# Optimization experiments

Measured on AMD Instinct MI355X. Metric: run time of the kernel, lower is better.

## Reference

```python
import jax, jax.numpy as jnp
import numpy as np

B = 8192
G = 30            # max_grid_size
C = 10            # num_colors
IN = G * G * C    # 9000 encoder input
HID = 128         # encoder hidden
ADIM = 128        # answer_dim
ZDIM = 64         # latent_dim
GF = 16           # grid_feature_dim
RHID = 64         # refiner / selector hidden
NT = 64           # num_templates
T = 3             # num_cycles
TAU = 1.0         # gumbel-softmax temperature


def _gelu(x):
    return jax.nn.gelu(x, approximate=False)  # torch nn.GELU default = exact erf


def setup_inputs() -> dict:
    key = jax.random.key(0)
    ks = jax.random.split(key, 32)
    s = 0.02
    inp = {
        "grid": jax.random.randint(ks[0], (B, G, G), 0, C, dtype=jnp.int64),
        "grid_features": jax.random.normal(ks[1], (B, GF), jnp.float32),
        "gumbel": jax.random.gumbel(ks[2], (B, NT), jnp.float32),
        # encoder (TinyMLPMixer)
        "enc_w1": jax.random.normal(ks[3], (IN, HID), jnp.float32) * s,
        "enc_b1": jnp.zeros((HID,), jnp.float32),
        "enc_w2": jax.random.normal(ks[4], (HID, HID), jnp.float32) * s,
        "enc_b2": jnp.zeros((HID,), jnp.float32),
        "wy": jax.random.normal(ks[5], (HID, ADIM), jnp.float32) * s,
        "by": jnp.zeros((ADIM,), jnp.float32),
        "wz": jax.random.normal(ks[6], (HID, ZDIM), jnp.float32) * s,
        "bz": jnp.zeros((ZDIM,), jnp.float32),
        # refine_z: [y,z,gf] (208) -> 64 -> ZDIM
        "rz_w1": jax.random.normal(ks[7], (ADIM + ZDIM + GF, RHID), jnp.float32) * s,
        "rz_b1": jnp.zeros((RHID,), jnp.float32),
        "rz_w2": jax.random.normal(ks[8], (RHID, ZDIM), jnp.float32) * s,
        "rz_b2": jnp.zeros((ZDIM,), jnp.float32),
        # refine_y: [z,y,gf] (208) -> 64 -> ADIM
        "ry_w1": jax.random.normal(ks[9], (ZDIM + ADIM + GF, RHID), jnp.float32) * s,
        "ry_b1": jnp.zeros((RHID,), jnp.float32),
        "ry_w2": jax.random.normal(ks[10], (RHID, ADIM), jnp.float32) * s,
        "ry_b2": jnp.zeros((ADIM,), jnp.float32),
        # formula selector: ADIM -> 64 -> NT
        "sel_w1": jax.random.normal(ks[11], (ADIM, RHID), jnp.float32) * s,
        "sel_b1": jnp.zeros((RHID,), jnp.float32),
        "sel_w2": jax.random.normal(ks[12], (RHID, NT), jnp.float32) * s,
        "sel_b2": jnp.zeros((NT,), jnp.float32),
    }
    return inp


def _mlp2(x, w1, b1, w2, b2):
    return _gelu(x @ w1 + b1) @ w2 + b2


def reference(grid, grid_features, gumbel,
              enc_w1, enc_b1, enc_w2, enc_b2, wy, by, wz, bz,
              rz_w1, rz_b1, rz_w2, rz_b2, ry_w1, ry_b1, ry_w2, ry_b2,
              sel_w1, sel_b1, sel_w2, sel_b2):
    # --- TinyMLPMixer encoder ---
    x = jax.nn.one_hot(grid, C, dtype=jnp.float32).reshape(grid.shape[0], -1)  # [B, 9000]
    h = _gelu(x @ enc_w1 + enc_b1)
    h = _gelu(h @ enc_w2 + enc_b2)
    y = h @ wy + by   # [B, ADIM]
    z = h @ wz + bz   # [B, ZDIM]

    def refine_z(y, z):
        return _mlp2(jnp.concatenate([y, z, grid_features], axis=-1), rz_w1, rz_b1, rz_w2, rz_b2)

    def refine_y(y, z):
        return _mlp2(jnp.concatenate([z, y, grid_features], axis=-1), ry_w1, ry_b1, ry_w2, ry_b2)

    # --- recursive refinement: T-1 no-grad cycles, final cycle with grads ---
    for _ in range(T - 1):
        z = jax.lax.stop_gradient(refine_z(y, z))
        y = jax.lax.stop_gradient(refine_y(y, z))
    z = refine_z(y, z)
    y = refine_y(y, z)

    # --- TinyFormulaSelector (Gumbel-Softmax, soft, noise passed in) ---
    logits = _mlp2(y, sel_w1, sel_b1, sel_w2, sel_b2)  # [B, NT]
    selection = jax.nn.softmax((logits + gumbel) / TAU, axis=-1)
    return selection
```

## Files before the change

kernel.cpp:

```cpp
#include <hip/hip_runtime.h>

typedef _Float16 f16;
typedef f16 h8 __attribute__((ext_vector_type(8)));
typedef float f32x4 __attribute__((ext_vector_type(4)));
typedef unsigned int uint;
typedef unsigned char uchar;

#define BM 32
#define KS_E 284
#define CSTR 920

#define SH 136
#define SAZ 232
#define SLOG 68

#define N_W1B (8*KS_E*512)
#define OW2   0
#define OWY   16384
#define OWZ   32768
#define ORZ1  40960
#define ORZ2  55296
#define ORY1  59392
#define ORY2  73728
#define OS1   81920
#define OS2   90112
#define N_SMH 94208

__device__ __forceinline__ float geluf(float x){
  return 0.5f * x * (1.0f + erff(x * 0.70710678118654752f));
}

#define MFMA16(a,b,c) __builtin_amdgcn_mfma_f32_16x16x32_f16(a, b, c, 0, 0, 0)

__device__ __forceinline__ f32x4 mfma8(uint2 a, uint2 b, f32x4 c){
  union { uint2 u; long long l; } ua, ub;
  ua.u = a; ub.u = b;
  return __builtin_amdgcn_mfma_f32_16x16x32_fp8_fp8(ua.l, ub.l, c, 0, 0, 0);
}

__device__ __forceinline__ f32x4 mfma_tile(const f16* __restrict__ act, int strideH,
                                           const f16* __restrict__ Wbase,
                                           int nks, f32x4 acc, int lane){
  #pragma unroll
  for (int ks = 0; ks < nks; ++ks){
    h8 a = *(const h8*)(act + (lane&15)*strideH + ks*32 + (lane>>4)*8);
    h8 b = *(const h8*)(Wbase + ks*512 + lane*8);
    acc = MFMA16(a, b, acc);
  }
  return acc;
}

__device__ __forceinline__ f32x4 cinit(const float* __restrict__ bias, int Nb, int lane){
  float v = bias[Nb + (lane&15)];
  f32x4 c; c[0]=v; c[1]=v; c[2]=v; c[3]=v;
  return c;
}

__device__ __forceinline__ void storeC16(f16* __restrict__ dst, int stride, int Nb,
                                         f32x4 c, int lane, bool dogelu){
  int col = Nb + (lane&15);
  int r0  = (lane>>4)*4;
  #pragma unroll
  for (int r = 0; r < 4; ++r){
    float v = c[r];
    if (dogelu) v = geluf(v);
    dst[(r0+r)*stride + col] = (f16)v;
  }
}

__global__ void prep_kernel(const float* __restrict__ w1,
  const float* __restrict__ w2, const float* __restrict__ wy, const float* __restrict__ wz,
  const float* __restrict__ rz1, const float* __restrict__ rz2,
  const float* __restrict__ ry1, const float* __restrict__ ry2,
  const float* __restrict__ sel1, const float* __restrict__ sel2, f16* __restrict__ ws)
{
  int idx = blockIdx.x * 256 + threadIdx.x;
  uchar* w8 = (uchar*)ws;
  if (idx < 9000*128){
    int row = idx >> 7;
    int n   = idx & 127;
    int p   = row / 10;
    int c   = row - p*10;
    int k   = 904*c + p;
    int nt  = n >> 4;
    int ks  = k >> 5;
    int lane = (((k>>3)&3)<<4) | (n&15);
    uint pk = __builtin_amdgcn_cvt_pk_fp8_f32(w1[idx], 0.f, 0, false);
    w8[((size_t)(nt*KS_E + ks)<<9) + (lane<<3) + (k&7)] = (uchar)(pk & 255u);
    return;
  }
  int i2 = idx - 9000*128;
  if (i2 < 11264){
    int k, n;
    if (i2 < 5120){
      int c = i2 >> 9, rest = i2 & 511;
      k = 904*c + 900 + (rest >> 7);
      n = rest & 127;
    } else {
      int j = i2 - 5120;
      k = 9040 + (j >> 7);
      n = j & 127;
    }
    int nt = n >> 4, ks = k >> 5;
    int lane = (((k>>3)&3)<<4) | (n&15);
    w8[((size_t)(nt*KS_E + ks)<<9) + (lane<<3) + (k&7)] = (uchar)0;
    return;
  }
  int r = i2 - 11264;
  if (r >= N_SMH) return;
  f16* smw = (f16*)(w8 + N_W1B);
  const float* src; int Ksrc, N, KS, off, perm = 0;
  if      (r < OWY) { src=w2;   Ksrc=128; N=128; KS=4; off=OW2; }
  else if (r < OWZ) { src=wy;   Ksrc=128; N=128; KS=4; off=OWY; }
  else if (r < ORZ1){ src=wz;   Ksrc=128; N=64;  KS=4; off=OWZ; }
  else if (r < ORZ2){ src=rz1;  Ksrc=208; N=64;  KS=7; off=ORZ1; }
  else if (r < ORY1){ src=rz2;  Ksrc=64;  N=64;  KS=2; off=ORZ2; }
  else if (r < ORY2){ src=ry1;  Ksrc=208; N=64;  KS=7; off=ORY1; perm=1; }
  else if (r < OS1) { src=ry2;  Ksrc=64;  N=128; KS=2; off=ORY2; }
  else if (r < OS2) { src=sel1; Ksrc=128; N=64;  KS=4; off=OS1; }
  else              { src=sel2; Ksrc=64;  N=64;  KS=2; off=OS2; }
  int l    = r - off;
  int e    = l & 7;
  int lane = (l >> 3) & 63;
  int frag = l >> 9;
  int kst  = frag % KS;
  int nt   = frag / KS;
  int k    = kst*32 + (lane>>4)*8 + e;
  int o    = nt*16 + (lane&15);
  float v = 0.f;
  if (perm){
    int sr = (k < 128) ? 64 + k : (k < 192) ? k - 128 : (k < 208) ? k : -1;
    if (sr >= 0) v = src[sr*N + o];
  } else if (k < Ksrc) v = src[k*N + o];
  smw[r] = (f16)v;
}

extern "C" __global__ __launch_bounds__(512, 1) void enc_kernel(
  const int* __restrict__ grd, const float* __restrict__ b1,
  const f16* __restrict__ ws, f16* hbuf)
{
  __shared__ __align__(16) char colL[32*CSTR];

  const int t  = threadIdx.x;
  const int s0 = blockIdx.x * BM;
  const int lane = t & 63;
  const int w    = t >> 6;

  {
    const uint4* gv = (const uint4*)(grd + (size_t)s0 * 900);
    #pragma unroll
    for (int it = 0; it < 15; ++it){
      int idx4 = it*512 + t;
      if (idx4 < 7200){
        uint4 v = gv[idx4];
        uint pk = (v.x & 255u) | ((v.y & 255u) << 8) | ((v.z & 255u) << 16) | ((v.w & 255u) << 24);
        uint s  = (uint)(idx4 * 9321u) >> 21;
        uint p4 = (uint)idx4 - s * 225u;
        *(uint*)(colL + s*CSTR + p4*4) = pk;
      }
    }
  }
  __syncthreads();

  const char* colRowA = colL + (lane & 15) * CSTR;
  const char* colRowB = colRowA + 16 * CSTR;
  const char* Wp = (const char*)ws + (size_t)(w * KS_E) * 512 + lane*8;

  f32x4 acc0 = {0.f,0.f,0.f,0.f};
  f32x4 acc1 = {0.f,0.f,0.f,0.f};

  uint2 q0 = *(const uint2*)(Wp);
  uint2 q1 = *(const uint2*)(Wp + 512);
  uint2 q2 = *(const uint2*)(Wp + 1024);
  uint2 q3 = *(const uint2*)(Wp + 1536);
  uint k0 = (uint)((lane >> 4) * 8);

#define ESTEP(Q, PFIDX) { \
    uint q = k0 >> 3; \
    uint c = (q * 2320u) >> 18; \
    uint p0 = (q - 113u * c) << 3; \
    uint2 wvA = *(const uint2*)(colRowA + p0); \
    uint2 wvB = *(const uint2*)(colRowB + p0); \
    uint cc4 = c * 0x01010101u; \
    uint2 a0, a1; \
    a0.x = (0x10101010u - (wvA.x ^ cc4)) & 0x10101010u; \
    a0.y = (0x10101010u - (wvA.y ^ cc4)) & 0x10101010u; \
    a1.x = (0x10101010u - (wvB.x ^ cc4)) & 0x10101010u; \
    a1.y = (0x10101010u - (wvB.y ^ cc4)) & 0x10101010u; \
    acc0 = mfma8(a0, Q, acc0); \
    acc1 = mfma8(a1, Q, acc1); \
    Q = *(const uint2*)(Wp + (size_t)(PFIDX)*512); \
    k0 += 32; }
#define ETAIL(Q) { \
    uint q = k0 >> 3; \
    uint c = (q * 2320u) >> 18; \
    uint p0 = (q - 113u * c) << 3; \
    uint2 wvA = *(const uint2*)(colRowA + p0); \
    uint2 wvB = *(const uint2*)(colRowB + p0); \
    uint cc4 = c * 0x01010101u; \
    uint2 a0, a1; \
    a0.x = (0x10101010u - (wvA.x ^ cc4)) & 0x10101010u; \
    a0.y = (0x10101010u - (wvA.y ^ cc4)) & 0x10101010u; \
    a1.x = (0x10101010u - (wvB.x ^ cc4)) & 0x10101010u; \
    a1.y = (0x10101010u - (wvB.y ^ cc4)) & 0x10101010u; \
    acc0 = mfma8(a0, Q, acc0); \
    acc1 = mfma8(a1, Q, acc1); \
    k0 += 32; }

  #pragma unroll 2
  for (int it = 0; it < 70; ++it){
    ESTEP(q0, it*4 + 4)
    ESTEP(q1, it*4 + 5)
    ESTEP(q2, it*4 + 6)
    ESTEP(q3, it*4 + 7)
  }
  ETAIL(q0) ETAIL(q1) ETAIL(q2) ETAIL(q3)
#undef ESTEP
#undef ETAIL

  {
    int col = w*16 + (lane & 15);
    float bb = b1[col];
    int r0 = (lane >> 4) * 4;
    #pragma unroll
    for (int r = 0; r < 4; ++r){
      hbuf[(size_t)(s0 + r0 + r)*128 + col]      = (f16)geluf(acc0[r]*32.0f + bb);
      hbuf[(size_t)(s0 + 16 + r0 + r)*128 + col] = (f16)geluf(acc1[r]*32.0f + bb);
    }
  }
}

extern "C" __global__ __launch_bounds__(256, 2) void phases_kernel(
  const float* __restrict__ gfeat, const float* __restrict__ gum,
  const float* __restrict__ b2, const float* __restrict__ by, const float* __restrict__ bz,
  const float* __restrict__ rzb1, const float* __restrict__ rzb2,
  const float* __restrict__ ryb1, const float* __restrict__ ryb2,
  const float* __restrict__ sb1, const float* __restrict__ sb2,
  const f16* __restrict__ ws, const f16* hbuf, float* out)
{
  __shared__ __align__(16) f16 Hb[16*SH];
  __shared__ __align__(16) f16 Bb[16*SH];
  __shared__ __align__(16) f16 Az[16*SAZ];
  __shared__ __align__(16) float Lb[16*SLOG];

  const int t  = threadIdx.x;
  const int s0 = blockIdx.x * 16;
  const int lane  = t & 63;
  const int ns    = t >> 6;
  const int slane = t >> 4;
  const int flane = t & 15;

  {
    h8 hv = *(const h8*)(hbuf + (size_t)s0*128 + t*8);
    *(h8*)(Hb + (t>>4)*SH + (t&15)*8) = hv;
    Az[slane*SAZ + 192 + flane] = (f16)gfeat[(size_t)(s0 + slane)*16 + flane];
    Az[slane*SAZ + 208 + flane] = (f16)0.f;
  }
  __syncthreads();

  const f16* SMW = (const f16*)((const char*)ws + N_W1B);

  {
    f32x4 c0 = cinit(b2, ns*32,      lane);
    f32x4 c1 = cinit(b2, ns*32 + 16, lane);
    c0 = mfma_tile(Hb, SH, SMW + OW2 + (ns*2+0)*4*512, 4, c0, lane);
    c1 = mfma_tile(Hb, SH, SMW + OW2 + (ns*2+1)*4*512, 4, c1, lane);
    storeC16(Bb, SH, ns*32,      c0, lane, true);
    storeC16(Bb, SH, ns*32 + 16, c1, lane, true);
  }
  __syncthreads();

  {
    f32x4 y0 = cinit(by, ns*32,      lane);
    f32x4 y1 = cinit(by, ns*32 + 16, lane);
    f32x4 z0 = cinit(bz, ns*16,      lane);
    y0 = mfma_tile(Bb, SH, SMW + OWY + (ns*2+0)*4*512, 4, y0, lane);
    y1 = mfma_tile(Bb, SH, SMW + OWY + (ns*2+1)*4*512, 4, y1, lane);
    z0 = mfma_tile(Bb, SH, SMW + OWZ + ns*4*512,       4, z0, lane);
    storeC16(Az, SAZ, ns*32,       y0, lane, false);
    storeC16(Az, SAZ, ns*32 + 16,  y1, lane, false);
    storeC16(Az, SAZ, 128 + ns*16, z0, lane, false);
  }
  __syncthreads();

  #pragma unroll 1
  for (int cyc = 0; cyc < 3; ++cyc){
    {
      f32x4 h0 = cinit(rzb1, ns*16, lane);
      h0 = mfma_tile(Az, SAZ, SMW + ORZ1 + ns*7*512, 7, h0, lane);
      storeC16(Bb, SH, ns*16, h0, lane, true);
    }
    __syncthreads();
    {
      f32x4 z = cinit(rzb2, ns*16, lane);
      z = mfma_tile(Bb, SH, SMW + ORZ2 + ns*2*512, 2, z, lane);
      storeC16(Az, SAZ, 128 + ns*16, z, lane, false);
    }
    __syncthreads();
    {
      f32x4 h1 = cinit(ryb1, ns*16, lane);
      h1 = mfma_tile(Az, SAZ, SMW + ORY1 + ns*7*512, 7, h1, lane);
      storeC16(Bb, SH, ns*16, h1, lane, true);
    }
    __syncthreads();
    {
      f32x4 y0 = cinit(ryb2, ns*32,      lane);
      f32x4 y1 = cinit(ryb2, ns*32 + 16, lane);
      y0 = mfma_tile(Bb, SH, SMW + ORY2 + (ns*2+0)*2*512, 2, y0, lane);
      y1 = mfma_tile(Bb, SH, SMW + ORY2 + (ns*2+1)*2*512, 2, y1, lane);
      storeC16(Az, SAZ, ns*32,      y0, lane, false);
      storeC16(Az, SAZ, ns*32 + 16, y1, lane, false);
    }
    __syncthreads();
  }

  {
    f32x4 s1 = cinit(sb1, ns*16, lane);
    s1 = mfma_tile(Az, SAZ, SMW + OS1 + ns*4*512, 4, s1, lane);
    storeC16(Bb, SH, ns*16, s1, lane, true);
  }
  __syncthreads();
  {
    f32x4 lg = cinit(sb2, ns*16, lane);
    lg = mfma_tile(Bb, SH, SMW + OS2 + ns*2*512, 2, lg, lane);
    int col = ns*16 + (lane & 15);
    int r0  = (lane >> 4) * 4;
    #pragma unroll
    for (int rr = 0; rr < 4; ++rr)
      Lb[(r0+rr)*SLOG + col] = lg[rr] + gum[(size_t)(s0 + r0 + rr)*64 + col];
  }
  __syncthreads();

  {
    const float* row = Lb + slane*SLOG;
    float m = -3.0e38f;
    #pragma unroll
    for (int k4 = 0; k4 < 16; ++k4){
      float4 v = *(const float4*)(row + k4*4);
      m = fmaxf(m, fmaxf(fmaxf(v.x,v.y), fmaxf(v.z,v.w)));
    }
    float ssum = 0.f;
    #pragma unroll
    for (int k4 = 0; k4 < 16; ++k4){
      float4 v = *(const float4*)(row + k4*4);
      ssum += __expf(v.x-m)+__expf(v.y-m)+__expf(v.z-m)+__expf(v.w-m);
    }
    float inv = 1.0f / ssum;
    const size_t gsamp = (size_t)(s0 + slane);
    #pragma unroll
    for (int j = 0; j < 4; ++j){
      int o = flane + 16*j;
      out[gsamp*64 + o] = __expf(row[o]-m) * inv;
    }
  }
}

extern "C" void kernel_launch(void* const* d_in, const int* in_sizes, int n_in,
                              void* d_out, int out_size, void* d_ws, size_t ws_size,
                              hipStream_t stream) {
  const int*   grd   = (const int*)d_in[0];
  const float* gfeat = (const float*)d_in[1];
  const float* gum   = (const float*)d_in[2];
  const float* w1    = (const float*)d_in[3];
  const float* b1    = (const float*)d_in[4];
  const float* w2    = (const float*)d_in[5];
  const float* b2    = (const float*)d_in[6];
  const float* wy    = (const float*)d_in[7];
  const float* byb   = (const float*)d_in[8];
  const float* wz    = (const float*)d_in[9];
  const float* bz    = (const float*)d_in[10];
  const float* rz1   = (const float*)d_in[11];
  const float* rzb1  = (const float*)d_in[12];
  const float* rz2   = (const float*)d_in[13];
  const float* rzb2  = (const float*)d_in[14];
  const float* ry1   = (const float*)d_in[15];
  const float* ryb1  = (const float*)d_in[16];
  const float* ry2   = (const float*)d_in[17];
  const float* ryb2  = (const float*)d_in[18];
  const float* sel1  = (const float*)d_in[19];
  const float* sb1   = (const float*)d_in[20];
  const float* sel2  = (const float*)d_in[21];
  const float* sb2   = (const float*)d_in[22];

  f16* ws = (f16*)d_ws;
  f16* hbuf = (f16*)d_out;
  float* outp = (float*)d_out;

  const int prep_total = 9000*128 + 11264 + N_SMH;
  prep_kernel<<<prep_total/256, 256, 0, stream>>>(
      w1, w2, wy, wz, rz1, rz2, ry1, ry2, sel1, sel2, ws);

  enc_kernel<<<8192/BM, 512, 0, stream>>>(grd, b1, ws, hbuf);

  phases_kernel<<<8192/16, 256, 0, stream>>>(
      gfeat, gum, b2, byb, bz, rzb1, rzb2, ryb1, ryb2, sb1, sb2, ws, hbuf, outp);
}
```

Before: 52.53 us.

## Split encoder K dimension across two blocks with fp32 partials reduced in phases kernel

The encoder's K loop is split into two halves, padded to 288 k-steps. Each half runs in its own block, so 512 blocks launch instead of 256, which fills more CUs on the MI355X. The fp32 partial sums go to workspace, and the phases kernel adds them, applies bias and GELU, then converts to fp16. This trades extra global traffic and a reduction for more parallelism. It falls back to the old path when the workspace is too small.

```diff
diff --git a/kernel.cpp b/kernel.cpp
--- a/kernel.cpp
+++ b/kernel.cpp
@@ -7,7 +7,8 @@
 typedef unsigned char uchar;
 
 #define BM 32
-#define KS_E 284
+#define KS_E 288
+#define KHB 144
 #define CSTR 920
 
 #define SH 136
@@ -25,6 +26,9 @@
 #define OS1   81920
 #define OS2   90112
 #define N_SMH 94208
+#define PART_OFF (2u<<20)
+#define PART_ELEMS (8192*128)
+#define WS_NEED ((10ull)<<20)
 
 __device__ __forceinline__ float geluf(float x){
   return 0.5f * x * (1.0f + erff(x * 0.70710678118654752f));
@@ -90,7 +94,7 @@
     return;
   }
   int i2 = idx - 9000*128;
-  if (i2 < 11264){
+  if (i2 < 27648){
     int k, n;
     if (i2 < 5120){
       int c = i2 >> 9, rest = i2 & 511;
@@ -106,7 +110,7 @@
     w8[((size_t)(nt*KS_E + ks)<<9) + (lane<<3) + (k&7)] = (uchar)0;
     return;
   }
-  int r = i2 - 11264;
+  int r = i2 - 27648;
   if (r >= N_SMH) return;
   f16* smw = (f16*)(w8 + N_W1B);
   const float* src; int Ksrc, N, KS, off, perm = 0;
@@ -135,14 +139,17 @@
   smw[r] = (f16)v;
 }
 
-extern "C" __global__ __launch_bounds__(512, 1) void enc_kernel(
+template<int NITER, bool F32OUT>
+__global__ __launch_bounds__(512, 1) void enc_t(
   const int* __restrict__ grd, const float* __restrict__ b1,
-  const f16* __restrict__ ws, f16* hbuf)
+  const f16* __restrict__ ws, f16* __restrict__ hbuf, float* __restrict__ part)
 {
   __shared__ __align__(16) char colL[32*CSTR];
 
   const int t  = threadIdx.x;
-  const int s0 = blockIdx.x * BM;
+  const int bid = blockIdx.x;
+  const int s0 = (F32OUT ? (bid >> 1) : bid) * BM;
+  const int kh = F32OUT ? (bid & 1) : 0;
   const int lane = t & 63;
   const int w    = t >> 6;
 
@@ -164,7 +171,7 @@
 
   const char* colRowA = colL + (lane & 15) * CSTR;
   const char* colRowB = colRowA + 16 * CSTR;
-  const char* Wp = (const char*)ws + (size_t)(w * KS_E) * 512 + lane*8;
+  const char* Wp = (const char*)ws + ((size_t)(w * KS_E) + (size_t)kh * KHB) * 512 + lane*8;
 
   f32x4 acc0 = {0.f,0.f,0.f,0.f};
   f32x4 acc1 = {0.f,0.f,0.f,0.f};
@@ -173,7 +180,7 @@
   uint2 q1 = *(const uint2*)(Wp + 512);
   uint2 q2 = *(const uint2*)(Wp + 1024);
   uint2 q3 = *(const uint2*)(Wp + 1536);
-  uint k0 = (uint)((lane >> 4) * 8);
+  uint k0 = (uint)(kh * (KHB*32)) + (uint)((lane >> 4) * 8);
 
 #define ESTEP(Q, PFIDX) { \
     uint q = k0 >> 3; \
@@ -208,7 +215,7 @@
     k0 += 32; }
 
   #pragma unroll 2
-  for (int it = 0; it < 70; ++it){
+  for (int it = 0; it < NITER; ++it){
     ESTEP(q0, it*4 + 4)
     ESTEP(q1, it*4 + 5)
     ESTEP(q2, it*4 + 6)
@@ -218,7 +225,16 @@
 #undef ESTEP
 #undef ETAIL
 
-  {
+  if (F32OUT){
+    float* P = part + (size_t)kh * PART_ELEMS;
+    int col = w*16 + (lane & 15);
+    int r0 = (lane >> 4) * 4;
+    #pragma unroll
+    for (int r = 0; r < 4; ++r){
+      P[(size_t)(s0 + r0 + r)*128 + col]      = acc0[r];
+      P[(size_t)(s0 + 16 + r0 + r)*128 + col] = acc1[r];
+    }
+  } else {
     int col = w*16 + (lane & 15);
     float bb = b1[col];
     int r0 = (lane >> 4) * 4;
@@ -230,13 +246,16 @@
   }
 }
 
-extern "C" __global__ __launch_bounds__(256, 2) void phases_kernel(
+template<bool SPLIT>
+__global__ __launch_bounds__(256, 2) void phases_t(
   const float* __restrict__ gfeat, const float* __restrict__ gum,
-  const float* __restrict__ b2, const float* __restrict__ by, const float* __restrict__ bz,
+  const float* __restrict__ b1, const float* __restrict__ b2,
+  const float* __restrict__ by, const float* __restrict__ bz,
   const float* __restrict__ rzb1, const float* __restrict__ rzb2,
   const float* __restrict__ ryb1, const float* __restrict__ ryb2,
   const float* __restrict__ sb1, const float* __restrict__ sb2,
-  const f16* __restrict__ ws, const f16* hbuf, float* out)
+  const f16* __restrict__ ws, const f16* __restrict__ hbuf,
+  const float* __restrict__ part, float* __restrict__ out)
 {
   __shared__ __align__(16) f16 Hb[16*SH];
   __shared__ __align__(16) f16 Bb[16*SH];
@@ -251,8 +270,19 @@
   const int flane = t & 15;
 
   {
-    h8 hv = *(const h8*)(hbuf + (size_t)s0*128 + t*8);
-    *(h8*)(Hb + (t>>4)*SH + (t&15)*8) = hv;
+    int ss = t >> 4, c8 = (t & 15) * 8;
+    if (SPLIT){
+      const float* p0 = part + (size_t)(s0 + ss)*128 + c8;
+      const float* p1 = p0 + PART_ELEMS;
+      h8 hv;
+      #pragma unroll
+      for (int j = 0; j < 8; ++j)
+        hv[j] = (f16)geluf((p0[j] + p1[j]) * 32.0f + b1[c8 + j]);
+      *(h8*)(Hb + ss*SH + c8) = hv;
+    } else {
+      h8 hv = *(const h8*)(hbuf + (size_t)s0*128 + t*8);
+      *(h8*)(Hb + ss*SH + c8) = hv;
+    }
     Az[slane*SAZ + 192 + flane] = (f16)gfeat[(size_t)(s0 + slane)*16 + flane];
     Az[slane*SAZ + 208 + flane] = (f16)0.f;
   }
@@ -383,15 +413,24 @@
   const float* sb2   = (const float*)d_in[22];
 
   f16* ws = (f16*)d_ws;
+  float* part = (float*)((char*)d_ws + PART_OFF);
   f16* hbuf = (f16*)d_out;
   float* outp = (float*)d_out;
 
-  const int prep_total = 9000*128 + 11264 + N_SMH;
+  const int prep_total = 9000*128 + 27648 + N_SMH;
   prep_kernel<<<prep_total/256, 256, 0, stream>>>(
       w1, w2, wy, wz, rz1, rz2, ry1, ry2, sel1, sel2, ws);
 
-  enc_kernel<<<8192/BM, 512, 0, stream>>>(grd, b1, ws, hbuf);
-
-  phases_kernel<<<8192/16, 256, 0, stream>>>(
-      gfeat, gum, b2, byb, bz, rzb1, rzb2, ryb1, ryb2, sb1, sb2, ws, hbuf, outp);
-}
+  const bool split = (ws_size >= WS_NEED);
+  if (split){
+    enc_t<KHB/4 - 1, true><<<512, 512, 0, stream>>>(grd, b1, ws, nullptr, part);
+    phases_t<true><<<8192/16, 256, 0, stream>>>(
+        gfeat, gum, b1, b2, byb, bz, rzb1, rzb2, ryb1, ryb2, sb1, sb2,
+        ws, nullptr, part, outp);
+  } else {
+    enc_t<70, false><<<8192/BM, 512, 0, stream>>>(grd, b1, ws, hbuf, nullptr);
+    phases_t<false><<<8192/16, 256, 0, stream>>>(
+        gfeat, gum, b1, b2, byb, bz, rzb1, rzb2, ryb1, ryb2, sb1, sb2,
+        ws, hbuf, nullptr, outp);
+  }
+}
```

After: 60.79 us. +15.7%, slower.
